# Optimization experiments

Hardware: AMD Instinct MI355X
Metric: run time of the kernel (lower is better)

Reference implementation:

```python
import jax, jax.numpy as jnp
import numpy as np

D_MODEL = 1024
N_HEADS = 16
B, T = 2, 2048


def setup_inputs() -> dict:
    key = jax.random.key(0)
    kx, kqkv, ko = jax.random.split(key, 3)
    x = jax.random.normal(kx, (B, T, D_MODEL), dtype=jnp.float32)
    # flax Linear default init (lecun_normal ~ scaled); plain scaled normal is fine for a baseline
    Wqkv = jax.random.normal(kqkv, (D_MODEL, 3 * D_MODEL), dtype=jnp.float32) / np.sqrt(D_MODEL)
    Wo = jax.random.normal(ko, (D_MODEL, D_MODEL), dtype=jnp.float32) / np.sqrt(D_MODEL)
    return {"x": x, "Wqkv": Wqkv, "Wo": Wo}


def reference(x, Wqkv, Wo):
    Bx, Tx, C = x.shape
    H = N_HEADS
    Hd = C // H
    scale = C ** (-0.5)  # NOTE: module scales by d_model**-0.5, not head_dim**-0.5
    qkv = x @ Wqkv  # [B, T, 3C]
    q, k, v = jnp.split(qkv, 3, axis=-1)
    q = q.reshape(Bx, Tx, H, Hd).transpose(0, 2, 1, 3)  # [B,H,T,Hd]
    k = k.reshape(Bx, Tx, H, Hd).transpose(0, 2, 1, 3)
    v = v.reshape(Bx, Tx, H, Hd).transpose(0, 2, 1, 3)
    attn = jnp.einsum('bhid,bhjd->bhij', q, k) * scale  # [B,H,T,T]
    mask = jnp.tril(jnp.ones((Tx, Tx), dtype=jnp.bool_))
    attn = jnp.where(mask[None, None], attn, jnp.finfo(attn.dtype).min)
    attn = jax.nn.softmax(attn.astype(jnp.float32), axis=-1).astype(attn.dtype)
    out = jnp.einsum('bhij,bhjd->bhid', attn, v)  # [B,H,T,Hd]
    out = out.transpose(0, 2, 1, 3).reshape(Bx, Tx, C)
    return out @ Wo
```

## Files before the change

### kernel.cpp

```cpp
#include <hip/hip_runtime.h>
#include <cstdint>
#include <math.h>

#define D_MODEL 1024
#define N_HEADS 16
#define HEAD_DIM 64
#define BB 2
#define TT 2048
#define QSCALE 0.04508422002778011f
#define MSTATIC 12.0f

typedef float f32x4 __attribute__((ext_vector_type(4)));
typedef __bf16 bf16x8 __attribute__((ext_vector_type(8)));

__device__ inline ushort f2bf(float f) {
    union { float f; uint32_t u; } c; c.f = f;
    uint32_t u = c.u;
    uint32_t r = (u + 0x7FFFu + ((u >> 16) & 1u)) >> 16;
    return (ushort)r;
}
__device__ inline ushort f2bf_hw(float f) {
    __bf16 h = (__bf16)f;
    return __builtin_bit_cast(ushort, h);
}

__device__ inline void load_lds16(const ushort* g, ushort* lds_uniform_base) {
    __builtin_amdgcn_global_load_lds(
        (const __attribute__((address_space(1))) uint32_t*)g,
        (__attribute__((address_space(3))) uint32_t*)lds_uniform_base, 16, 0, 0);
}

__global__ __launch_bounds__(256) void conv_x(
    const float4* __restrict__ in, ushort4* __restrict__ out, int n4)
{
    int i = blockIdx.x * 256 + threadIdx.x;
    if (i < n4) {
        float4 v = in[i];
        ushort4 u;
        u.x = f2bf(v.x); u.y = f2bf(v.y); u.z = f2bf(v.z); u.w = f2bf(v.w);
        out[i] = u;
    }
}

__global__ __launch_bounds__(256) void transpose_f32_bf16(
    const float* __restrict__ in, ushort* __restrict__ out, int R, int C)
{
    __shared__ ushort tile[32][33];
    int tx = threadIdx.x;
    int ty = threadIdx.y;
    int c0 = blockIdx.x * 32;
    int r0 = blockIdx.y * 32;
#pragma unroll
    for (int i = 0; i < 32; i += 8)
        tile[ty + i][tx] = f2bf(in[(size_t)(r0 + ty + i) * C + (c0 + tx)]);
    __syncthreads();
#pragma unroll
    for (int i = 0; i < 32; i += 8)
        out[(size_t)(c0 + ty + i) * R + (r0 + tx)] = tile[tx][ty + i];
}

__global__ __launch_bounds__(256) void transpose_v_bf16(
    const ushort* __restrict__ in, ushort* __restrict__ out)
{
    int z = blockIdx.z;
    const ushort* ip = in + (size_t)z * TT * HEAD_DIM;
    ushort* op = out + (size_t)z * TT * HEAD_DIM;
    __shared__ ushort tile[32][33];
    int tx = threadIdx.x, ty = threadIdx.y;
    int d0 = blockIdx.x * 32;
    int t0 = blockIdx.y * 32;
#pragma unroll
    for (int i = 0; i < 32; i += 8)
        tile[ty + i][tx] = ip[(size_t)(t0 + ty + i) * HEAD_DIM + d0 + tx];
    __syncthreads();
#pragma unroll
    for (int i = 0; i < 32; i += 8)
        op[(size_t)(d0 + ty + i) * TT + t0 + tx] = tile[tx][ty + i];
}

__device__ inline void gemm128_mainloop(
    const ushort* __restrict__ A, const ushort* __restrict__ BT,
    int rowBase, int colBase, ushort* Al, ushort* Bl,
    f32x4 acc[4][4], int wave, int lane)
{
    const int K = D_MODEL;
    int lr = lane & 15, quad = lane >> 4;
    int lrow = lane >> 2;
    int kq = lane & 3;
    int mq = (wave >> 1) * 64, nq = (wave & 1) * 64;

    const ushort* gA0 = A + (size_t)(rowBase + wave * 32 + lrow) * K + kq * 8;
    const ushort* gA1 = gA0 + (size_t)16 * K;
    const ushort* gB0 = BT + (size_t)(colBase + wave * 32 + lrow) * K + kq * 8;
    const ushort* gB1 = gB0 + (size_t)16 * K;
    ushort* lA0 = Al + (wave * 32) * 32;
    ushort* lA1 = Al + (wave * 32 + 16) * 32;
    ushort* lB0 = Bl + (wave * 32) * 32;
    ushort* lB1 = Bl + (wave * 32 + 16) * 32;

    for (int kt = 0; kt < K / 32; ++kt) {
        __syncthreads();
        int ko = kt * 32;
        load_lds16(gA0 + ko, lA0);
        load_lds16(gA1 + ko, lA1);
        load_lds16(gB0 + ko, lB0);
        load_lds16(gB1 + ko, lB1);
        __syncthreads();
        bf16x8 af[4], bf[4];
#pragma unroll
        for (int mi = 0; mi < 4; ++mi)
            af[mi] = *(const bf16x8*)(Al + (mq + mi * 16 + lr) * 32 + quad * 8);
#pragma unroll
        for (int ni = 0; ni < 4; ++ni)
            bf[ni] = *(const bf16x8*)(Bl + (nq + ni * 16 + lr) * 32 + quad * 8);
#pragma unroll
        for (int mi = 0; mi < 4; ++mi)
#pragma unroll
            for (int ni = 0; ni < 4; ++ni)
                acc[mi][ni] = __builtin_amdgcn_mfma_f32_16x16x32_bf16(
                    af[mi], bf[ni], acc[mi][ni], 0, 0, 0);
    }
}

__global__ __launch_bounds__(256) void gemm_qkv(
    const ushort* __restrict__ A, const ushort* __restrict__ BT,
    ushort* __restrict__ Qo, ushort* __restrict__ Ko, ushort* __restrict__ Vo)
{
    __shared__ ushort Al[128 * 32];
    __shared__ ushort Bl[128 * 32];
    int tid = threadIdx.x;
    int wave = tid >> 6, lane = tid & 63;
    int lr = lane & 15, quad = lane >> 4;
    int rowBase = blockIdx.y * 128;
    int colBase = blockIdx.x * 128;
    f32x4 acc[4][4] = {};
    gemm128_mainloop(A, BT, rowBase, colBase, Al, Bl, acc, wave, lane);

    int mq = (wave >> 1) * 64, nq = (wave & 1) * 64;
#pragma unroll
    for (int ni = 0; ni < 4; ++ni) {
        int n = colBase + nq + ni * 16 + lr;
        int s = n >> 10;
        int cc = n & 1023;
        int h = cc >> 6, d = cc & 63;
        ushort* dst = (s == 0) ? Qo : (s == 1 ? Ko : Vo);
        float scale = (s == 0) ? QSCALE : 1.0f;
#pragma unroll
        for (int mi = 0; mi < 4; ++mi) {
#pragma unroll
            for (int i = 0; i < 4; ++i) {
                int m = rowBase + mq + mi * 16 + quad * 4 + i;
                int b = m >> 11, t = m & 2047;
                int bh = b * N_HEADS + h;
                dst[((size_t)bh * TT + t) * HEAD_DIM + d] = f2bf(acc[mi][ni][i] * scale);
            }
        }
    }
}

__global__ __launch_bounds__(256) void gemm_plain(
    const ushort* __restrict__ A, const ushort* __restrict__ BT,
    float* __restrict__ O, int N)
{
    const int K = D_MODEL;
    __shared__ ushort Al[128 * 32];
    __shared__ ushort Bl[64 * 32];
    int tid = threadIdx.x;
    int wave = tid >> 6, lane = tid & 63;
    int lr = lane & 15, quad = lane >> 4;
    int lrow = lane >> 2, kq = lane & 3;
    int rowBase = blockIdx.y * 128;
    int colBase = blockIdx.x * 64;
    int mq = (wave >> 1) * 64, nq = (wave & 1) * 32;

    const ushort* gA0 = A + (size_t)(rowBase + wave * 32 + lrow) * K + kq * 8;
    const ushort* gA1 = gA0 + (size_t)16 * K;
    const ushort* gB0 = BT + (size_t)(colBase + wave * 32 + lrow) * K + kq * 8;
    const ushort* gB1 = gB0 + (size_t)16 * K;
    ushort* lA0 = Al + (wave * 32) * 32;
    ushort* lA1 = Al + (wave * 32 + 16) * 32;
    ushort* lB0 = Bl + (wave * 32) * 32;
    ushort* lB1 = Bl + (wave * 32 + 16) * 32;

    f32x4 acc[4][2] = {};
    for (int kt = 0; kt < K / 32; ++kt) {
        __syncthreads();
        int ko = kt * 32;
        load_lds16(gA0 + ko, lA0);
        load_lds16(gA1 + ko, lA1);
        if (wave < 2) {
            load_lds16(gB0 + ko, lB0);
            load_lds16(gB1 + ko, lB1);
        }
        __syncthreads();
        bf16x8 af[4], bf[2];
#pragma unroll
        for (int mi = 0; mi < 4; ++mi)
            af[mi] = *(const bf16x8*)(Al + (mq + mi * 16 + lr) * 32 + quad * 8);
#pragma unroll
        for (int ni = 0; ni < 2; ++ni)
            bf[ni] = *(const bf16x8*)(Bl + (nq + ni * 16 + lr) * 32 + quad * 8);
#pragma unroll
        for (int mi = 0; mi < 4; ++mi)
#pragma unroll
            for (int ni = 0; ni < 2; ++ni)
                acc[mi][ni] = __builtin_amdgcn_mfma_f32_16x16x32_bf16(
                    af[mi], bf[ni], acc[mi][ni], 0, 0, 0);
    }

#pragma unroll
    for (int mi = 0; mi < 4; ++mi)
#pragma unroll
        for (int ni = 0; ni < 2; ++ni) {
            int n = colBase + nq + ni * 16 + lr;
#pragma unroll
            for (int i = 0; i < 4; ++i) {
                int m = rowBase + mq + mi * 16 + quad * 4 + i;
                O[(size_t)m * N + n] = acc[mi][ni][i];
            }
        }
}

__global__ __launch_bounds__(256) void attn_flash(
    const ushort* __restrict__ Q,
    const ushort* __restrict__ K,
    const ushort* __restrict__ VT,
    ushort* __restrict__ AO)
{
    int bid = blockIdx.x;
    int bh  = bid & 31;
    int idx = bid >> 5;
    int qi  = (idx < 8) ? idx : (23 - idx);
    int tid = threadIdx.x;
    int wave = tid >> 6, lane = tid & 63;
    int quad = lane >> 4, lr = lane & 15;
    int qb = qi * 128;
    int qw = qb + wave * 32;

    const ushort* Qb = Q  + (size_t)bh * TT * HEAD_DIM;
    const ushort* Kb = K  + (size_t)bh * TT * HEAD_DIM;
    const ushort* Vb = VT + (size_t)bh * HEAD_DIM * TT;

    __shared__ ushort Kl[2][32 * 64];
    __shared__ ushort Vl[2][64 * 32];
    __shared__ ushort pbuf[4][32][40];
    ushort (*P)[40] = pbuf[wave];

    int krow = lane >> 3, kchunk = lane & 7;
    int vrow = lane >> 2, vchunk = lane & 3;
    const ushort* gK = Kb + (size_t)(wave * 8 + krow) * HEAD_DIM + kchunk * 8;
    const ushort* gV = Vb + (size_t)(wave * 16 + vrow) * TT + vchunk * 8;

    bf16x8 qa[2][2];
#pragma unroll
    for (int r = 0; r < 2; ++r)
#pragma unroll
        for (int s = 0; s < 2; ++s)
            qa[r][s] = *(const bf16x8*)(Qb + (size_t)(qw + r * 16 + lr) * HEAD_DIM
                                           + s * 32 + quad * 8);

    f32x4 o[2][4] = {};
    f32x4 l[2] = {};

    bf16x8 ones;
#pragma unroll
    for (int j = 0; j < 8; ++j) ones[j] = (__bf16)1.0f;

    int myktiles = (qw >> 5) + 1;
    int blocktiles = (qb >> 5) + 4;

    for (int kt = 0; kt < blocktiles; ++kt) {
        int buf = kt & 1;
        __syncthreads();
        load_lds16(gK + (size_t)(kt * 32) * HEAD_DIM, &Kl[buf][wave * 512]);
        load_lds16(gV + kt * 32,                      &Vl[buf][wave * 512]);
        __syncthreads();

        if (kt < myktiles) {
            bf16x8 kb[2][2], vb[4];
#pragma unroll
            for (int c = 0; c < 2; ++c)
#pragma unroll
                for (int s = 0; s < 2; ++s)
                    kb[c][s] = *(const bf16x8*)&Kl[buf][(c * 16 + lr) * 64 + s * 32 + quad * 8];
#pragma unroll
            for (int d = 0; d < 4; ++d)
                vb[d] = *(const bf16x8*)&Vl[buf][(d * 16 + lr) * 32 + quad * 8];

            f32x4 sc[2][2];
#pragma unroll
            for (int r = 0; r < 2; ++r)
#pragma unroll
                for (int c = 0; c < 2; ++c)
#pragma unroll
                    for (int i = 0; i < 4; ++i) sc[r][c][i] = -MSTATIC;
#pragma unroll
            for (int r = 0; r < 2; ++r)
#pragma unroll
                for (int c = 0; c < 2; ++c) {
                    sc[r][c] = __builtin_amdgcn_mfma_f32_16x16x32_bf16(qa[r][0], kb[c][0], sc[r][c], 0, 0, 0);
                    sc[r][c] = __builtin_amdgcn_mfma_f32_16x16x32_bf16(qa[r][1], kb[c][1], sc[r][c], 0, 0, 0);
                }
            if (kt == myktiles - 1) {
#pragma unroll
                for (int r = 0; r < 2; ++r)
#pragma unroll
                    for (int c = 0; c < 2; ++c)
#pragma unroll
                        for (int i = 0; i < 4; ++i)
                            if (c * 16 + lr > r * 16 + quad * 4 + i) sc[r][c][i] = -3e38f;
            }

#pragma unroll
            for (int r = 0; r < 2; ++r)
#pragma unroll
                for (int c = 0; c < 2; ++c)
#pragma unroll
                    for (int i = 0; i < 4; ++i)
                        P[r * 16 + quad * 4 + i][c * 16 + lr] =
                            f2bf_hw(__builtin_amdgcn_exp2f(sc[r][c][i]));

#pragma unroll
            for (int r = 0; r < 2; ++r) {
                bf16x8 pa = *(const bf16x8*)&P[r * 16 + lr][quad * 8];
                l[r] = __builtin_amdgcn_mfma_f32_16x16x32_bf16(pa, ones, l[r], 0, 0, 0);
#pragma unroll
                for (int d = 0; d < 4; ++d)
                    o[r][d] = __builtin_amdgcn_mfma_f32_16x16x32_bf16(pa, vb[d], o[r][d], 0, 0, 0);
            }
        }
    }

    int b = bh >> 4, h = bh & 15;
#pragma unroll
    for (int r = 0; r < 2; ++r) {
        f32x4 rl;
#pragma unroll
        for (int i = 0; i < 4; ++i) rl[i] = 1.0f / l[r][i];
#pragma unroll
        for (int d = 0; d < 4; ++d)
#pragma unroll
            for (int i = 0; i < 4; ++i) {
                int row = qw + r * 16 + quad * 4 + i;
                AO[((size_t)(b * TT + row)) * D_MODEL + h * HEAD_DIM + d * 16 + lr] =
                    f2bf(o[r][d][i] * rl[i]);
            }
    }
}

extern "C" void kernel_launch(void* const* d_in, const int* in_sizes, int n_in,
                              void* d_out, int out_size, void* d_ws, size_t ws_size,
                              hipStream_t stream)
{
    (void)in_sizes; (void)n_in; (void)out_size; (void)ws_size;
    const float* x    = (const float*)d_in[0];
    const float* Wqkv = (const float*)d_in[1];
    const float* Wo   = (const float*)d_in[2];
    float* out = (float*)d_out;

    char* ws = (char*)d_ws;
    size_t off = 0;
    ushort* WqkvT = (ushort*)(ws + off); off += (size_t)3 * D_MODEL * D_MODEL * 2;
    ushort* WoT   = (ushort*)(ws + off); off += (size_t)D_MODEL * D_MODEL * 2;
    ushort* xb    = (ushort*)(ws + off); off += (size_t)BB * TT * D_MODEL * 2;
    ushort* Qd    = (ushort*)(ws + off); off += (size_t)BB * D_MODEL * TT * 2;
    ushort* Kd    = (ushort*)(ws + off); off += (size_t)BB * D_MODEL * TT * 2;
    ushort* Vd    = (ushort*)(ws + off); off += (size_t)BB * D_MODEL * TT * 2;
    ushort* VTd   = (ushort*)(ws + off); off += (size_t)BB * D_MODEL * TT * 2;
    ushort* AO    = (ushort*)(ws + off); off += (size_t)BB * TT * D_MODEL * 2;

    int n4 = BB * TT * D_MODEL / 4;
    conv_x<<<dim3(n4 / 256), 256, 0, stream>>>(
        (const float4*)x, (ushort4*)xb, n4);

    transpose_f32_bf16<<<dim3(3 * D_MODEL / 32, D_MODEL / 32), dim3(32, 8), 0, stream>>>(
        Wqkv, WqkvT, D_MODEL, 3 * D_MODEL);
    transpose_f32_bf16<<<dim3(D_MODEL / 32, D_MODEL / 32), dim3(32, 8), 0, stream>>>(
        Wo, WoT, D_MODEL, D_MODEL);

    gemm_qkv<<<dim3(3 * D_MODEL / 128, BB * TT / 128), 256, 0, stream>>>(
        xb, WqkvT, Qd, Kd, Vd);

    transpose_v_bf16<<<dim3(HEAD_DIM / 32, TT / 32, BB * N_HEADS), dim3(32, 8), 0, stream>>>(
        Vd, VTd);

    attn_flash<<<dim3(512), 256, 0, stream>>>(Qd, Kd, VTd, AO);

    gemm_plain<<<dim3(D_MODEL / 64, BB * TT / 128), 256, 0, stream>>>(
        AO, WoT, out, D_MODEL);
}
```

Measured before the change: 214.5 us.

## Fuse prep kernels and restructure attention to transposed-score MFMA without LDS staging

Merges the x conversion and both weight transposes into a single prep launch. Rewrites the attention kernel to compute S^T = K·Q^T so the exp'd probabilities land directly in MFMA operand layout, removing the per-wave LDS P buffer, the ones-MFMA row sum, and the shared K/V LDS tiles and block barriers. Each wave now streams K/V straight from global memory for only its own causal tiles, and the output goes through an LDS staging buffer so it can be written with coalesced 16-byte stores. The trade-off is that waves in a block no longer share K/V loads, which increases global/L2 traffic and relies on the cache.

```diff
diff --git a/kernel.cpp b/kernel.cpp
--- a/kernel.cpp
+++ b/kernel.cpp
@@ -12,6 +12,7 @@
 
 typedef float f32x4 __attribute__((ext_vector_type(4)));
 typedef __bf16 bf16x8 __attribute__((ext_vector_type(8)));
+typedef __bf16 bf16x4 __attribute__((ext_vector_type(4)));
 
 __device__ inline ushort f2bf(float f) {
     union { float f; uint32_t u; } c; c.f = f;
@@ -30,26 +31,33 @@
         (__attribute__((address_space(3))) uint32_t*)lds_uniform_base, 16, 0, 0);
 }
 
-__global__ __launch_bounds__(256) void conv_x(
-    const float4* __restrict__ in, ushort4* __restrict__ out, int n4)
-{
-    int i = blockIdx.x * 256 + threadIdx.x;
-    if (i < n4) {
-        float4 v = in[i];
+__global__ __launch_bounds__(256) void prep(
+    const float4* __restrict__ xin, ushort4* __restrict__ xb,
+    const float* __restrict__ Wqkv, ushort* __restrict__ WqkvT,
+    const float* __restrict__ Wo, ushort* __restrict__ WoT)
+{
+    int bid = blockIdx.x;
+    int tid = threadIdx.x;
+    if (bid < 4096) {
+        int i = bid * 256 + tid;
+        float4 v = xin[i];
         ushort4 u;
         u.x = f2bf(v.x); u.y = f2bf(v.y); u.z = f2bf(v.z); u.w = f2bf(v.w);
-        out[i] = u;
-    }
-}
-
-__global__ __launch_bounds__(256) void transpose_f32_bf16(
-    const float* __restrict__ in, ushort* __restrict__ out, int R, int C)
-{
+        xb[i] = u;
+        return;
+    }
     __shared__ ushort tile[32][33];
-    int tx = threadIdx.x;
-    int ty = threadIdx.y;
-    int c0 = blockIdx.x * 32;
-    int r0 = blockIdx.y * 32;
+    int tx = tid & 31, ty = tid >> 5;
+    const float* in; ushort* out; int R, C, c0, r0;
+    if (bid < 7168) {
+        int b2 = bid - 4096;
+        in = Wqkv; out = WqkvT; R = D_MODEL; C = 3 * D_MODEL;
+        c0 = (b2 % 96) * 32; r0 = (b2 / 96) * 32;
+    } else {
+        int b3 = bid - 7168;
+        in = Wo; out = WoT; R = D_MODEL; C = D_MODEL;
+        c0 = (b3 % 32) * 32; r0 = (b3 / 32) * 32;
+    }
 #pragma unroll
     for (int i = 0; i < 32; i += 8)
         tile[ty + i][tx] = f2bf(in[(size_t)(r0 + ty + i) * C + (c0 + tx)]);
@@ -234,118 +242,113 @@
     int tid = threadIdx.x;
     int wave = tid >> 6, lane = tid & 63;
     int quad = lane >> 4, lr = lane & 15;
-    int qb = qi * 128;
-    int qw = qb + wave * 32;
+    int qw = qi * 128 + wave * 32;
 
     const ushort* Qb = Q  + (size_t)bh * TT * HEAD_DIM;
     const ushort* Kb = K  + (size_t)bh * TT * HEAD_DIM;
     const ushort* Vb = VT + (size_t)bh * HEAD_DIM * TT;
 
-    __shared__ ushort Kl[2][32 * 64];
-    __shared__ ushort Vl[2][64 * 32];
-    __shared__ ushort pbuf[4][32][40];
-    ushort (*P)[40] = pbuf[wave];
-
-    int krow = lane >> 3, kchunk = lane & 7;
-    int vrow = lane >> 2, vchunk = lane & 3;
-    const ushort* gK = Kb + (size_t)(wave * 8 + krow) * HEAD_DIM + kchunk * 8;
-    const ushort* gV = Vb + (size_t)(wave * 16 + vrow) * TT + vchunk * 8;
-
-    bf16x8 qa[2][2];
-#pragma unroll
-    for (int r = 0; r < 2; ++r)
+    __shared__ ushort obuf[4][32 * 64];
+
+    bf16x8 qb[2][2];
+#pragma unroll
+    for (int qg = 0; qg < 2; ++qg)
 #pragma unroll
         for (int s = 0; s < 2; ++s)
-            qa[r][s] = *(const bf16x8*)(Qb + (size_t)(qw + r * 16 + lr) * HEAD_DIM
-                                           + s * 32 + quad * 8);
-
-    f32x4 o[2][4] = {};
-    f32x4 l[2] = {};
-
-    bf16x8 ones;
-#pragma unroll
-    for (int j = 0; j < 8; ++j) ones[j] = (__bf16)1.0f;
-
-    int myktiles = (qw >> 5) + 1;
-    int blocktiles = (qb >> 5) + 4;
-
-    for (int kt = 0; kt < blocktiles; ++kt) {
-        int buf = kt & 1;
-        __syncthreads();
-        load_lds16(gK + (size_t)(kt * 32) * HEAD_DIM, &Kl[buf][wave * 512]);
-        load_lds16(gV + kt * 32,                      &Vl[buf][wave * 512]);
-        __syncthreads();
-
-        if (kt < myktiles) {
-            bf16x8 kb[2][2], vb[4];
+            qb[qg][s] = *(const bf16x8*)(Qb + (size_t)(qw + qg * 16 + lr) * HEAD_DIM
+                                            + s * 32 + quad * 8);
+
+    f32x4 oT[2][4] = {};
+    float lsum[2] = {0.f, 0.f};
+
+    int ktiles = (qw >> 5) + 1;
+    for (int kt = 0; kt < ktiles; ++kt) {
+        int k0 = kt << 5;
+        bf16x8 ka[2][2];
+#pragma unroll
+        for (int c = 0; c < 2; ++c)
+#pragma unroll
+            for (int s = 0; s < 2; ++s)
+                ka[c][s] = *(const bf16x8*)(Kb + (size_t)(k0 + c * 16 + lr) * HEAD_DIM
+                                               + s * 32 + quad * 8);
+        bf16x8 va[4];
+#pragma unroll
+        for (int dg = 0; dg < 4; ++dg) {
+            bf16x4 lo = *(const bf16x4*)(Vb + (size_t)(dg * 16 + lr) * TT + k0 + quad * 4);
+            bf16x4 hi = *(const bf16x4*)(Vb + (size_t)(dg * 16 + lr) * TT + k0 + 16 + quad * 4);
+#pragma unroll
+            for (int j = 0; j < 4; ++j) { va[dg][j] = lo[j]; va[dg][4 + j] = hi[j]; }
+        }
+
+        f32x4 st[2][2];
+#pragma unroll
+        for (int qg = 0; qg < 2; ++qg)
 #pragma unroll
             for (int c = 0; c < 2; ++c)
 #pragma unroll
-                for (int s = 0; s < 2; ++s)
-                    kb[c][s] = *(const bf16x8*)&Kl[buf][(c * 16 + lr) * 64 + s * 32 + quad * 8];
-#pragma unroll
-            for (int d = 0; d < 4; ++d)
-                vb[d] = *(const bf16x8*)&Vl[buf][(d * 16 + lr) * 32 + quad * 8];
-
-            f32x4 sc[2][2];
-#pragma unroll
-            for (int r = 0; r < 2; ++r)
+                for (int i = 0; i < 4; ++i) st[qg][c][i] = -MSTATIC;
+#pragma unroll
+        for (int qg = 0; qg < 2; ++qg)
+#pragma unroll
+            for (int c = 0; c < 2; ++c) {
+                st[qg][c] = __builtin_amdgcn_mfma_f32_16x16x32_bf16(ka[c][0], qb[qg][0], st[qg][c], 0, 0, 0);
+                st[qg][c] = __builtin_amdgcn_mfma_f32_16x16x32_bf16(ka[c][1], qb[qg][1], st[qg][c], 0, 0, 0);
+            }
+        if (kt == ktiles - 1) {
+#pragma unroll
+            for (int qg = 0; qg < 2; ++qg)
 #pragma unroll
                 for (int c = 0; c < 2; ++c)
 #pragma unroll
-                    for (int i = 0; i < 4; ++i) sc[r][c][i] = -MSTATIC;
-#pragma unroll
-            for (int r = 0; r < 2; ++r)
-#pragma unroll
-                for (int c = 0; c < 2; ++c) {
-                    sc[r][c] = __builtin_amdgcn_mfma_f32_16x16x32_bf16(qa[r][0], kb[c][0], sc[r][c], 0, 0, 0);
-                    sc[r][c] = __builtin_amdgcn_mfma_f32_16x16x32_bf16(qa[r][1], kb[c][1], sc[r][c], 0, 0, 0);
-                }
-            if (kt == myktiles - 1) {
-#pragma unroll
-                for (int r = 0; r < 2; ++r)
-#pragma unroll
-                    for (int c = 0; c < 2; ++c)
-#pragma unroll
-                        for (int i = 0; i < 4; ++i)
-                            if (c * 16 + lr > r * 16 + quad * 4 + i) sc[r][c][i] = -3e38f;
+                    for (int i = 0; i < 4; ++i)
+                        if (c * 16 + quad * 4 + i > qg * 16 + lr) st[qg][c][i] = -3e38f;
+        }
+
+#pragma unroll
+        for (int qg = 0; qg < 2; ++qg) {
+            bf16x8 pt;
+            float s0 = 0.f;
+#pragma unroll
+            for (int i = 0; i < 4; ++i) {
+                float e0 = __builtin_amdgcn_exp2f(st[qg][0][i]);
+                float e1 = __builtin_amdgcn_exp2f(st[qg][1][i]);
+                pt[i] = (__bf16)e0;
+                pt[4 + i] = (__bf16)e1;
+                s0 += e0 + e1;
             }
-
-#pragma unroll
-            for (int r = 0; r < 2; ++r)
-#pragma unroll
-                for (int c = 0; c < 2; ++c)
-#pragma unroll
-                    for (int i = 0; i < 4; ++i)
-                        P[r * 16 + quad * 4 + i][c * 16 + lr] =
-                            f2bf_hw(__builtin_amdgcn_exp2f(sc[r][c][i]));
-
-#pragma unroll
-            for (int r = 0; r < 2; ++r) {
-                bf16x8 pa = *(const bf16x8*)&P[r * 16 + lr][quad * 8];
-                l[r] = __builtin_amdgcn_mfma_f32_16x16x32_bf16(pa, ones, l[r], 0, 0, 0);
-#pragma unroll
-                for (int d = 0; d < 4; ++d)
-                    o[r][d] = __builtin_amdgcn_mfma_f32_16x16x32_bf16(pa, vb[d], o[r][d], 0, 0, 0);
-            }
-        }
+            lsum[qg] += s0;
+#pragma unroll
+            for (int dg = 0; dg < 4; ++dg)
+                oT[qg][dg] = __builtin_amdgcn_mfma_f32_16x16x32_bf16(va[dg], pt, oT[qg][dg], 0, 0, 0);
+        }
+    }
+
+#pragma unroll
+    for (int qg = 0; qg < 2; ++qg) {
+        lsum[qg] += __shfl_xor(lsum[qg], 16);
+        lsum[qg] += __shfl_xor(lsum[qg], 32);
     }
 
     int b = bh >> 4, h = bh & 15;
 #pragma unroll
-    for (int r = 0; r < 2; ++r) {
-        f32x4 rl;
-#pragma unroll
-        for (int i = 0; i < 4; ++i) rl[i] = 1.0f / l[r][i];
-#pragma unroll
-        for (int d = 0; d < 4; ++d)
-#pragma unroll
-            for (int i = 0; i < 4; ++i) {
-                int row = qw + r * 16 + quad * 4 + i;
-                AO[((size_t)(b * TT + row)) * D_MODEL + h * HEAD_DIM + d * 16 + lr] =
-                    f2bf(o[r][d][i] * rl[i]);
-            }
-    }
+    for (int qg = 0; qg < 2; ++qg) {
+        float rinv = 1.0f / lsum[qg];
+#pragma unroll
+        for (int dg = 0; dg < 4; ++dg) {
+            ushort4 w;
+            w.x = f2bf_hw(oT[qg][dg][0] * rinv);
+            w.y = f2bf_hw(oT[qg][dg][1] * rinv);
+            w.z = f2bf_hw(oT[qg][dg][2] * rinv);
+            w.w = f2bf_hw(oT[qg][dg][3] * rinv);
+            *(ushort4*)&obuf[wave][(qg * 16 + lr) * 64 + dg * 16 + quad * 4] = w;
+        }
+    }
+    int ql = lane >> 1, hf = lane & 1;
+    const ushort* src = &obuf[wave][ql * 64 + hf * 32];
+    ushort* dst = AO + (size_t)(b * TT + qw + ql) * D_MODEL + h * HEAD_DIM + hf * 32;
+#pragma unroll
+    for (int ch = 0; ch < 4; ++ch)
+        *(uint4*)(dst + ch * 8) = *(const uint4*)(src + ch * 8);
 }
 
 extern "C" void kernel_launch(void* const* d_in, const int* in_sizes, int n_in,
@@ -369,14 +372,8 @@
     ushort* VTd   = (ushort*)(ws + off); off += (size_t)BB * D_MODEL * TT * 2;
     ushort* AO    = (ushort*)(ws + off); off += (size_t)BB * TT * D_MODEL * 2;
 
-    int n4 = BB * TT * D_MODEL / 4;
-    conv_x<<<dim3(n4 / 256), 256, 0, stream>>>(
-        (const float4*)x, (ushort4*)xb, n4);
-
-    transpose_f32_bf16<<<dim3(3 * D_MODEL / 32, D_MODEL / 32), dim3(32, 8), 0, stream>>>(
-        Wqkv, WqkvT, D_MODEL, 3 * D_MODEL);
-    transpose_f32_bf16<<<dim3(D_MODEL / 32, D_MODEL / 32), dim3(32, 8), 0, stream>>>(
-        Wo, WoT, D_MODEL, D_MODEL);
+    prep<<<dim3(8192), 256, 0, stream>>>(
+        (const float4*)x, (ushort4*)xb, Wqkv, WqkvT, Wo, WoT);
 
     gemm_qkv<<<dim3(3 * D_MODEL / 128, BB * TT / 128), 256, 0, stream>>>(
         xb, WqkvT, Qd, Kd, Vd);
```

New measurement: 237.0 us. 1.1x slower.

## Merge prep kernels and use 64-key LDS tiles in flash attention

Applied to the files above, without the earlier changes.

Folds the x conversion and the two weight transposes into one prep kernel, which removes two launches. In attention, K and V are now staged in 64-key tiles with a chunk-major LDS layout, so two 32-key sub-steps run per barrier pair. The LDS buffer is no longer double-buffered, and the new layout changes the bank access pattern.

```diff
diff --git a/kernel.cpp b/kernel.cpp
--- a/kernel.cpp
+++ b/kernel.cpp
@@ -30,26 +30,33 @@
         (__attribute__((address_space(3))) uint32_t*)lds_uniform_base, 16, 0, 0);
 }
 
-__global__ __launch_bounds__(256) void conv_x(
-    const float4* __restrict__ in, ushort4* __restrict__ out, int n4)
-{
-    int i = blockIdx.x * 256 + threadIdx.x;
-    if (i < n4) {
-        float4 v = in[i];
+__global__ __launch_bounds__(256) void prep(
+    const float4* __restrict__ xin, ushort4* __restrict__ xb,
+    const float* __restrict__ Wqkv, ushort* __restrict__ WqkvT,
+    const float* __restrict__ Wo, ushort* __restrict__ WoT)
+{
+    int bid = blockIdx.x;
+    int tid = threadIdx.x;
+    if (bid < 4096) {
+        int i = bid * 256 + tid;
+        float4 v = xin[i];
         ushort4 u;
         u.x = f2bf(v.x); u.y = f2bf(v.y); u.z = f2bf(v.z); u.w = f2bf(v.w);
-        out[i] = u;
-    }
-}
-
-__global__ __launch_bounds__(256) void transpose_f32_bf16(
-    const float* __restrict__ in, ushort* __restrict__ out, int R, int C)
-{
+        xb[i] = u;
+        return;
+    }
     __shared__ ushort tile[32][33];
-    int tx = threadIdx.x;
-    int ty = threadIdx.y;
-    int c0 = blockIdx.x * 32;
-    int r0 = blockIdx.y * 32;
+    int tx = tid & 31, ty = tid >> 5;
+    const float* in; ushort* out; int R, C, c0, r0;
+    if (bid < 7168) {
+        int b2 = bid - 4096;
+        in = Wqkv; out = WqkvT; R = D_MODEL; C = 3 * D_MODEL;
+        c0 = (b2 % 96) * 32; r0 = (b2 / 96) * 32;
+    } else {
+        int b3 = bid - 7168;
+        in = Wo; out = WoT; R = D_MODEL; C = D_MODEL;
+        c0 = (b3 % 32) * 32; r0 = (b3 / 32) * 32;
+    }
 #pragma unroll
     for (int i = 0; i < 32; i += 8)
         tile[ty + i][tx] = f2bf(in[(size_t)(r0 + ty + i) * C + (c0 + tx)]);
@@ -241,15 +248,19 @@
     const ushort* Kb = K  + (size_t)bh * TT * HEAD_DIM;
     const ushort* Vb = VT + (size_t)bh * HEAD_DIM * TT;
 
-    __shared__ ushort Kl[2][32 * 64];
-    __shared__ ushort Vl[2][64 * 32];
+    __shared__ ushort Kl[8 * 64 * 8];
+    __shared__ ushort Vl[8 * 64 * 8];
     __shared__ ushort pbuf[4][32][40];
     ushort (*P)[40] = pbuf[wave];
 
-    int krow = lane >> 3, kchunk = lane & 7;
-    int vrow = lane >> 2, vchunk = lane & 3;
-    const ushort* gK = Kb + (size_t)(wave * 8 + krow) * HEAD_DIM + kchunk * 8;
-    const ushort* gV = Vb + (size_t)(wave * 16 + vrow) * TT + vchunk * 8;
+    const ushort* gK0 = Kb + (size_t)lane * HEAD_DIM + wave * 8;
+    const ushort* gK1 = Kb + (size_t)lane * HEAD_DIM + (wave + 4) * 8;
+    const ushort* gV0 = Vb + (size_t)lane * TT + wave * 8;
+    const ushort* gV1 = Vb + (size_t)lane * TT + 32 + wave * 8;
+    ushort* lK0 = Kl + wave * 512;
+    ushort* lK1 = Kl + (wave + 4) * 512;
+    ushort* lV0 = Vl + wave * 512;
+    ushort* lV1 = Vl + (wave + 4) * 512;
 
     bf16x8 qa[2][2];
 #pragma unroll
@@ -267,25 +278,34 @@
     for (int j = 0; j < 8; ++j) ones[j] = (__bf16)1.0f;
 
     int myktiles = (qw >> 5) + 1;
-    int blocktiles = (qb >> 5) + 4;
-
-    for (int kt = 0; kt < blocktiles; ++kt) {
-        int buf = kt & 1;
-        __syncthreads();
-        load_lds16(gK + (size_t)(kt * 32) * HEAD_DIM, &Kl[buf][wave * 512]);
-        load_lds16(gV + kt * 32,                      &Vl[buf][wave * 512]);
-        __syncthreads();
-
-        if (kt < myktiles) {
-            bf16x8 kb[2][2], vb[4];
+    int tiles64 = (qb >> 6) + 2;
+
+    for (int kt64 = 0; kt64 < tiles64; ++kt64) {
+        size_t koff = (size_t)kt64 * 64;
+        __syncthreads();
+        load_lds16(gK0 + koff * HEAD_DIM, lK0);
+        load_lds16(gK1 + koff * HEAD_DIM, lK1);
+        load_lds16(gV0 + koff, lV0);
+        load_lds16(gV1 + koff, lV1);
+        __syncthreads();
+
+#pragma unroll
+        for (int sub = 0; sub < 2; ++sub) {
+            int kt32 = kt64 * 2 + sub;
+            if (kt32 >= myktiles) break;
+
+            bf16x8 kb[2][2];
 #pragma unroll
             for (int c = 0; c < 2; ++c)
 #pragma unroll
                 for (int s = 0; s < 2; ++s)
-                    kb[c][s] = *(const bf16x8*)&Kl[buf][(c * 16 + lr) * 64 + s * 32 + quad * 8];
+                    kb[c][s] = *(const bf16x8*)&Kl[(((s * 4 + quad) * 64)
+                                 + sub * 32 + c * 16 + lr) * 8];
+            bf16x8 vb[4];
 #pragma unroll
             for (int d = 0; d < 4; ++d)
-                vb[d] = *(const bf16x8*)&Vl[buf][(d * 16 + lr) * 32 + quad * 8];
+                vb[d] = *(const bf16x8*)&Vl[(((sub * 4 + quad) * 64)
+                             + d * 16 + lr) * 8];
 
             f32x4 sc[2][2];
 #pragma unroll
@@ -301,7 +321,7 @@
                     sc[r][c] = __builtin_amdgcn_mfma_f32_16x16x32_bf16(qa[r][0], kb[c][0], sc[r][c], 0, 0, 0);
                     sc[r][c] = __builtin_amdgcn_mfma_f32_16x16x32_bf16(qa[r][1], kb[c][1], sc[r][c], 0, 0, 0);
                 }
-            if (kt == myktiles - 1) {
+            if (kt32 == myktiles - 1) {
 #pragma unroll
                 for (int r = 0; r < 2; ++r)
 #pragma unroll
@@ -369,14 +389,8 @@
     ushort* VTd   = (ushort*)(ws + off); off += (size_t)BB * D_MODEL * TT * 2;
     ushort* AO    = (ushort*)(ws + off); off += (size_t)BB * TT * D_MODEL * 2;
 
-    int n4 = BB * TT * D_MODEL / 4;
-    conv_x<<<dim3(n4 / 256), 256, 0, stream>>>(
-        (const float4*)x, (ushort4*)xb, n4);
-
-    transpose_f32_bf16<<<dim3(3 * D_MODEL / 32, D_MODEL / 32), dim3(32, 8), 0, stream>>>(
-        Wqkv, WqkvT, D_MODEL, 3 * D_MODEL);
-    transpose_f32_bf16<<<dim3(D_MODEL / 32, D_MODEL / 32), dim3(32, 8), 0, stream>>>(
-        Wo, WoT, D_MODEL, D_MODEL);
+    prep<<<dim3(8192), 256, 0, stream>>>(
+        (const float4*)x, (ushort4*)xb, Wqkv, WqkvT, Wo, WoT);
 
     gemm_qkv<<<dim3(3 * D_MODEL / 128, BB * TT / 128), 256, 0, stream>>>(
         xb, WqkvT, Qd, Kd, Vd);
```

After: 204.6 us. 4.6% less time.
